# Performance work log

Hardware: AMD Instinct MI355X
Metric: run time of the kernel (lower is better)

Reference implementation:

```python
import jax, jax.numpy as jnp
import numpy as np
from jax import lax

NK, NV, DK, DV, K, C = 16, 32, 128, 128, 4, 2048
KEY_DIM = NK * DK
VAL_DIM = NV * DV
CONV_DIM = 2 * KEY_DIM + VAL_DIM
EPS = 1e-6


def setup_inputs() -> dict:
    key = jax.random.key(0)
    ks = jax.random.split(key, 10)
    B, T = 2, 2048
    s = 0.02
    return {
        "x": jax.random.normal(ks[0], (B, T, C), jnp.float32),
        "input_pos": jnp.arange(T, dtype=jnp.int32),
        "W_qkv": jax.random.normal(ks[1], (CONV_DIM, C), jnp.float32) * s,
        "W_z": jax.random.normal(ks[2], (VAL_DIM, C), jnp.float32) * s,
        "W_b": jax.random.normal(ks[3], (NV, C), jnp.float32) * s,
        "W_a": jax.random.normal(ks[4], (NV, C), jnp.float32) * s,
        "conv_w": jax.random.normal(ks[5], (CONV_DIM, 1, K), jnp.float32) * 0.1,
        "dt_bias": jnp.ones((NV,), jnp.float32),
        "A_log": jnp.log(jax.random.uniform(ks[6], (NV,), jnp.float32, 1e-3, 16.0)),
        "norm_w": jnp.ones((DV,), jnp.float32),
        "W_out": jax.random.normal(ks[7], (C, VAL_DIM), jnp.float32) * s,
        "conv_state": jnp.zeros((B, CONV_DIM, K), jnp.float32),
        "recurrent_state": jnp.zeros((B, NV, DK, DV), jnp.float32),
    }


def reference(x, input_pos, W_qkv, W_z, W_b, W_a, conv_w, dt_bias, A_log,
              norm_w, W_out, conv_state, recurrent_state):
    B, T, _ = x.shape
    # reset cached state when starting a new sequence (input_pos[0] == 0)
    keep = 1.0 - (input_pos[0] == 0).astype(x.dtype)
    conv_state = conv_state * keep
    state0 = recurrent_state * keep

    qkv = jnp.einsum('btc,dc->btd', x, W_qkv)                      # [B,T,CONV_DIM]
    z = jnp.einsum('btc,dc->btd', x, W_z).reshape(B, T, NV, DV)
    beta = jax.nn.sigmoid(jnp.einsum('btc,hc->bth', x, W_b))       # [B,T,NV]
    a = jnp.einsum('btc,hc->bth', x, W_a)
    g = -jnp.exp(A_log) * jax.nn.softplus(a + dt_bias)             # [B,T,NV]

    # causal depthwise conv using cached conv_state as left context
    conv_in = jnp.concatenate([conv_state, qkv.transpose(0, 2, 1)], axis=-1)  # [B,D,K+T]
    conv_out = lax.conv_general_dilated(
        conv_in, conv_w, (1,), 'VALID',
        dimension_numbers=('NCH', 'OIH', 'NCH'),
        feature_group_count=CONV_DIM)
    qkv_c = jax.nn.silu(conv_out[:, :, -T:]).transpose(0, 2, 1)    # [B,T,CONV_DIM]

    q = qkv_c[..., :KEY_DIM].reshape(B, T, NK, DK)
    k = qkv_c[..., KEY_DIM:2 * KEY_DIM].reshape(B, T, NK, DK)
    v = qkv_c[..., 2 * KEY_DIM:].reshape(B, T, NV, DV)
    q = q / jnp.maximum(jnp.linalg.norm(q, axis=-1, keepdims=True), 1e-12)
    k = k / jnp.maximum(jnp.linalg.norm(k, axis=-1, keepdims=True), 1e-12)
    rep = NV // NK
    if rep > 1:
        q = jnp.repeat(q, rep, axis=2)
        k = jnp.repeat(k, rep, axis=2)

    # gated delta-rule recurrence over time
    def step(carry, xs):
        q_i, k_i, v_i, g_i, b_i = xs                               # [B,H,*]
        new = (jnp.exp(g_i)[..., None, None] * carry
               + b_i[..., None, None] * (k_i[..., :, None] * v_i[..., None, :]))
        out = jnp.einsum('bhk,bhkv->bhv', q_i, new)
        return new, out

    xs = (q.transpose(1, 0, 2, 3), k.transpose(1, 0, 2, 3),
          v.transpose(1, 0, 2, 3), g.transpose(1, 0, 2), beta.transpose(1, 0, 2))
    state, outs = lax.scan(step, state0, xs)
    o = outs.transpose(1, 0, 2, 3)                                 # [B,T,NV,DV]

    # gated RMSNorm (Mamba2-style): gate with silu(z), then RMS-normalize
    o = o * jax.nn.silu(z)
    var = jnp.mean(o * o, axis=-1, keepdims=True)
    o = o * lax.rsqrt(var + EPS) * norm_w
    return jnp.einsum('btd,cd->btc', o.reshape(B, T, VAL_DIM), W_out)
```

## Files before the change

kernel.cpp:

```cpp
#include <hip/hip_runtime.h>
#include <hip/hip_bf16.h>
#include <math.h>

#define NKH 16
#define NVH 32
#define DKD 128
#define DVD 128
#define CDIM 2048
#define KEY_DIM 2048
#define VAL_DIM 4096
#define CONV_DIM 8192
#define BB 2
#define TT 2048
#define MROWS 4096
#define CH 64
#define NCHUNK 32

typedef unsigned short u16;
typedef __bf16 bf16x8 __attribute__((ext_vector_type(8)));
typedef float f32x4 __attribute__((ext_vector_type(4)));

__device__ __forceinline__ u16 f2bf(float f) {
    union { float f; unsigned u; } a; a.f = f;
    unsigned u = a.u;
    u += 0x7fffu + ((u >> 16) & 1u);
    return (u16)(u >> 16);
}
__device__ __forceinline__ float bf2f(u16 h) {
    union { unsigned u; float f; } a; a.u = ((unsigned)h) << 16;
    return a.f;
}
union BF8 { bf16x8 v; uint2 u2[2]; uint4 u4; u16 s[8]; };
__device__ __forceinline__ bf16x8 lds_ld8(const u16* p) {
    BF8 t; t.u2[0] = *(const uint2*)p; t.u2[1] = *(const uint2*)(p + 4); return t.v;
}
__device__ __forceinline__ bf16x8 lds_ld16(const u16* p) {
    BF8 t; t.u4 = *(const uint4*)p; return t.v;
}
__device__ __forceinline__ void lds_st8(u16* p, uint4 v) {
    *(uint2*)p = make_uint2(v.x, v.y); *(uint2*)(p + 4) = make_uint2(v.z, v.w);
}

__global__ __launch_bounds__(256) void fill_kernel(float* __restrict__ p, float v, int n) {
    int i = blockIdx.x * 256 + threadIdx.x;
    if (i < n) p[i] = v;
}

__global__ __launch_bounds__(256) void cast_kernel(const float* __restrict__ src,
                                                   u16* __restrict__ dst, int n4) {
    int i = blockIdx.x * 256 + threadIdx.x;
    if (i >= n4) return;
    float4 v = ((const float4*)src)[i];
    ushort4 r;
    r.x = f2bf(v.x); r.y = f2bf(v.y); r.z = f2bf(v.z); r.w = f2bf(v.w);
    ((ushort4*)dst)[i] = r;
}

template<int OUT_BF16>
__global__ __launch_bounds__(256) void gemm_nt(const u16* __restrict__ A,
                                               const u16* __restrict__ Bm,
                                               void* __restrict__ Cv,
                                               int M, int N, int K) {
    __shared__ __align__(16) u16 As[128 * 64];
    __shared__ __align__(16) u16 Bs[128 * 64];
    const int tid  = threadIdx.x;
    const int lane = tid & 63;
    const int wave = tid >> 6;
    const int m0 = blockIdx.y * 128;
    const int n0 = blockIdx.x * 128;
    const int wm = (wave & 1) * 64;
    const int wn = (wave >> 1) * 64;
    const int l15  = lane & 15;
    const int quad = lane >> 4;

    f32x4 acc[4][4];
#pragma unroll
    for (int i = 0; i < 4; ++i)
#pragma unroll
        for (int j = 0; j < 4; ++j) acc[i][j] = (f32x4)0.0f;

    const int crow = tid >> 3;
    const int ccol = (tid & 7) * 8;

    for (int k0 = 0; k0 < K; k0 += 64) {
#pragma unroll
        for (int p = 0; p < 4; ++p) {
            int row = p * 32 + crow;
            const u16* ga = A + (size_t)(m0 + row) * K + k0 + ccol;
            char* la = (char*)As + (size_t)(p * 256 + (wave << 6)) * 16;
            __builtin_amdgcn_global_load_lds((const __attribute__((address_space(1))) void*)ga,
                                             (__attribute__((address_space(3))) void*)la, 16, 0, 0);
            const u16* gb = Bm + (size_t)(n0 + row) * K + k0 + ccol;
            char* lb = (char*)Bs + (size_t)(p * 256 + (wave << 6)) * 16;
            __builtin_amdgcn_global_load_lds((const __attribute__((address_space(1))) void*)gb,
                                             (__attribute__((address_space(3))) void*)lb, 16, 0, 0);
        }
        __syncthreads();
#pragma unroll
        for (int kk = 0; kk < 64; kk += 32) {
            bf16x8 af[4], bfr[4];
#pragma unroll
            for (int i = 0; i < 4; ++i) {
                af[i]  = *(const bf16x8*)&As[(wm + i * 16 + l15) * 64 + kk + quad * 8];
                bfr[i] = *(const bf16x8*)&Bs[(wn + i * 16 + l15) * 64 + kk + quad * 8];
            }
#pragma unroll
            for (int i = 0; i < 4; ++i)
#pragma unroll
                for (int j = 0; j < 4; ++j)
                    acc[i][j] = __builtin_amdgcn_mfma_f32_16x16x32_bf16(af[i], bfr[j], acc[i][j], 0, 0, 0);
        }
        __syncthreads();
    }
#pragma unroll
    for (int i = 0; i < 4; ++i) {
#pragma unroll
        for (int j = 0; j < 4; ++j) {
#pragma unroll
            for (int r = 0; r < 4; ++r) {
                int grow = m0 + wm + i * 16 + quad * 4 + r;
                int gcol = n0 + wn + j * 16 + l15;
                if (OUT_BF16) {
                    ((u16*)Cv)[(size_t)grow * N + gcol] = f2bf(acc[i][j][r]);
                } else {
                    ((float*)Cv)[(size_t)grow * N + gcol] = acc[i][j][r];
                }
            }
        }
    }
}

template<int OUT_BF16>
__global__ __launch_bounds__(512, 2) void gemm_nt_256(const u16* __restrict__ A,
                                                      const u16* __restrict__ Bm,
                                                      void* __restrict__ Cv,
                                                      int M, int N, int K) {
    __shared__ __align__(16) u16 sA[2][256 * 64];
    __shared__ __align__(16) u16 sB[2][256 * 64];
    const int tid  = threadIdx.x;
    const int lane = tid & 63;
    const int wave = tid >> 6;
    const int wr   = wave >> 2;
    const int wc   = wave & 3;
    const int l15  = lane & 15;
    const int quad = lane >> 4;
    const int m0 = blockIdx.y * 256;
    const int n0 = blockIdx.x * 256;

    f32x4 acc[8][4];
#pragma unroll
    for (int i = 0; i < 8; ++i)
#pragma unroll
        for (int j = 0; j < 4; ++j) acc[i][j] = (f32x4)0.0f;

    auto stage = [&](int buf, int kk0) {
#pragma unroll
        for (int p = 0; p < 4; ++p) {
            const int gbase = p * 512 + wave * 64;
            const int g   = gbase + lane;
            const int row = g >> 3;
            const int sc  = (g & 7) ^ (row & 7);
            const u16* ga = A + (size_t)(m0 + row) * K + kk0 + sc * 8;
            __builtin_amdgcn_global_load_lds(
                (const __attribute__((address_space(1))) void*)ga,
                (__attribute__((address_space(3))) void*)((char*)&sA[buf][0] + (size_t)gbase * 16),
                16, 0, 0);
            const u16* gb = Bm + (size_t)(n0 + row) * K + kk0 + sc * 8;
            __builtin_amdgcn_global_load_lds(
                (const __attribute__((address_space(1))) void*)gb,
                (__attribute__((address_space(3))) void*)((char*)&sB[buf][0] + (size_t)gbase * 16),
                16, 0, 0);
        }
    };

    const int NT = K >> 6;
    stage(0, 0);

    for (int T = 0; T < NT; ++T) {
        const int P = T & 1;
        __builtin_amdgcn_sched_barrier(0);
        if (T + 1 < NT) {
            stage(P ^ 1, (T + 1) << 6);
            asm volatile("s_waitcnt vmcnt(8)" ::: "memory");
        } else {
            asm volatile("s_waitcnt vmcnt(0)" ::: "memory");
        }
        __builtin_amdgcn_s_barrier();
        __builtin_amdgcn_sched_barrier(0);
#pragma unroll
        for (int kk = 0; kk < 2; ++kk) {
            bf16x8 af[8], bfv[4];
#pragma unroll
            for (int i = 0; i < 8; ++i) {
                int row = wr * 128 + i * 16 + l15;
                int slot = ((kk * 4 + quad) ^ (l15 & 7)) * 8;
                af[i] = lds_ld16(&sA[P][row * 64 + slot]);
            }
#pragma unroll
            for (int j = 0; j < 4; ++j) {
                int row = wc * 64 + j * 16 + l15;
                int slot = ((kk * 4 + quad) ^ (l15 & 7)) * 8;
                bfv[j] = lds_ld16(&sB[P][row * 64 + slot]);
            }
#pragma unroll
            for (int i = 0; i < 8; ++i)
#pragma unroll
                for (int j = 0; j < 4; ++j)
                    acc[i][j] = __builtin_amdgcn_mfma_f32_16x16x32_bf16(af[i], bfv[j], acc[i][j], 0, 0, 0);
        }
        __builtin_amdgcn_sched_barrier(0);
        __builtin_amdgcn_s_barrier();
    }

#pragma unroll
    for (int i = 0; i < 8; ++i) {
#pragma unroll
        for (int j = 0; j < 4; ++j) {
#pragma unroll
            for (int r = 0; r < 4; ++r) {
                int grow = m0 + wr * 128 + i * 16 + quad * 4 + r;
                int gcol = n0 + wc * 64 + j * 16 + l15;
                if (OUT_BF16) {
                    ((u16*)Cv)[(size_t)grow * N + gcol] = f2bf(acc[i][j][r]);
                } else {
                    ((float*)Cv)[(size_t)grow * N + gcol] = acc[i][j][r];
                }
            }
        }
    }
}

__global__ __launch_bounds__(256) void bg_epilogue(const float* __restrict__ scores,
                                                   const float* __restrict__ dt_bias,
                                                   const float* __restrict__ A_log,
                                                   float* __restrict__ beta,
                                                   float* __restrict__ g) {
    int i = blockIdx.x * 256 + threadIdx.x;
    int row = i >> 6, col = i & 63;
    float s = scores[(size_t)row * 128 + col];
    if (col < 32) {
        beta[(size_t)row * 32 + col] = 1.f / (1.f + __expf(-s));
    } else {
        int h = col - 32;
        float aa = s + dt_bias[h];
        float sp = (aa > 20.f) ? aa : log1pf(__expf(aa));
        g[(size_t)row * 32 + h] = -__expf(A_log[h]) * sp;
    }
}

__global__ __launch_bounds__(256) void conv_silu_kernel(const u16* __restrict__ qkv,
                                                        const float* __restrict__ conv_w,
                                                        const float* __restrict__ conv_state,
                                                        const int* __restrict__ input_pos,
                                                        u16* __restrict__ qkvc) {
    const int d   = blockIdx.x * 256 + threadIdx.x;
    const int row = blockIdx.y;
    const int t   = row & (TT - 1);
    const int b   = row >> 11;
    const float keep = (input_pos[0] == 0) ? 0.f : 1.f;
    float4 w = *(const float4*)&conv_w[(size_t)d * 4];
    float acc = 0.f;
#pragma unroll
    for (int j = 0; j < 4; ++j) {
        int u = t + j - 3;
        float v;
        if (u >= 0) v = bf2f(qkv[(size_t)(b * TT + u) * CONV_DIM + d]);
        else        v = keep * conv_state[((size_t)b * CONV_DIM + d) * 4 + (u + 4)];
        acc += (&w.x)[j] * v;
    }
    float s = acc / (1.f + __expf(-acc));
    qkvc[(size_t)row * CONV_DIM + d] = f2bf(s);
}

__global__ __launch_bounds__(256) void qknorm_kernel(u16* __restrict__ qkvc) {
    const int gid  = blockIdx.x * 4 + (threadIdx.x >> 6);
    const int lane = threadIdx.x & 63;
    const int row  = gid >> 5;
    const int h    = gid & 31;
    u16* p = qkvc + (size_t)row * CONV_DIM + h * 128;
    ushort2 vb = *(ushort2*)&p[lane * 2];
    float v0 = bf2f(vb.x), v1 = bf2f(vb.y);
    float ss = v0 * v0 + v1 * v1;
#pragma unroll
    for (int off = 32; off; off >>= 1) ss += __shfl_xor(ss, off);
    float scale = 1.f / fmaxf(sqrtf(ss), 1e-12f);
    ushort2 r;
    r.x = f2bf(v0 * scale);
    r.y = f2bf(v1 * scale);
    *(ushort2*)&p[lane * 2] = r;
}

__global__ __launch_bounds__(64) void gates_kernel(const float* __restrict__ g,
                                                   const float* __restrict__ beta_,
                                                   float* __restrict__ gcum,
                                                   float* __restrict__ qsb,
                                                   float* __restrict__ wkb,
                                                   float* __restrict__ dLb) {
    const int bh = blockIdx.x, c = blockIdx.y;
    const int b = bh >> 5, h = bh & 31;
    const int t = threadIdx.x;
    const int row = b * TT + c * CH + t;
    float G = g[(size_t)row * 32 + h];
#pragma unroll
    for (int off = 1; off < 64; off <<= 1) {
        float x = __shfl_up(G, off);
        if (t >= off) G += x;
    }
    float GL = __shfl(G, 63);
    int oidx = bh * TT + c * CH + t;
    gcum[oidx] = G;
    qsb[oidx] = __expf(G);
    wkb[oidx] = __expf(GL - G) * beta_[(size_t)row * 32 + h];
    if (t == 0) dLb[bh * NCHUNK + c] = __expf(GL);
}

__global__ __launch_bounds__(256) void ktrans_kernel(const u16* __restrict__ qkvc,
                                                     u16* __restrict__ kT) {
    const int id = blockIdx.x;
    const int tt = id & 31, dkh = (id >> 5) & 1, hk = (id >> 6) & 15, b = id >> 10;
    const int t0 = tt * 64, dk0 = dkh * 64;
    __shared__ __align__(16) u16 tile[64 * 68];
#pragma unroll
    for (int it = 0; it < 2; ++it) {
        int idx = it * 256 + threadIdx.x;
        int tl = idx >> 3, c8 = (idx & 7) * 8;
        uint4 v = *(const uint4*)&qkvc[(size_t)(b * TT + t0 + tl) * CONV_DIM + KEY_DIM + hk * 128 + dk0 + c8];
        lds_st8(&tile[tl * 68 + c8], v);
    }
    __syncthreads();
#pragma unroll
    for (int it = 0; it < 2; ++it) {
        int idx = it * 256 + threadIdx.x;
        int dkl = idx >> 3, t8 = (idx & 7) * 8;
        unsigned w[4];
#pragma unroll
        for (int p = 0; p < 4; ++p) {
            unsigned lo = tile[(t8 + 2 * p) * 68 + dkl];
            unsigned hi = tile[(t8 + 2 * p + 1) * 68 + dkl];
            w[p] = lo | (hi << 16);
        }
        *(uint4*)&kT[((size_t)((b * 16 + hk) * 128 + dk0 + dkl)) * TT + t0 + t8] =
            make_uint4(w[0], w[1], w[2], w[3]);
    }
}

__global__ __launch_bounds__(256) void chunk_state_kernel(const u16* __restrict__ qkvc,
                                                          const u16* __restrict__ kT,
                                                          const float* __restrict__ qsb,
                                                          const float* __restrict__ wkb,
                                                          const float* __restrict__ dLb,
                                                          const float* __restrict__ rec_state,
                                                          const int* __restrict__ input_pos,
                                                          u16* __restrict__ o) {
    const int b = blockIdx.x, h = blockIdx.y, dvs = blockIdx.z;
    const int tid = threadIdx.x, lane = tid & 63, wave = tid >> 6;
    const int l15 = lane & 15, quad = lane >> 4;
    const int hq = h >> 1, bh = b * 32 + h;
    const float keep = (input_pos[0] == 0) ? 0.f : 1.f;

    __shared__ __align__(16) u16 sQ[64 * 132];
    __shared__ __align__(16) u16 sKT[128 * 68];
    __shared__ __align__(16) u16 sR[32 * 132];
    __shared__ float sQS[64];

    f32x4 st[2][2];
#pragma unroll
    for (int i = 0; i < 2; ++i)
#pragma unroll
        for (int j = 0; j < 2; ++j)
#pragma unroll
            for (int r = 0; r < 4; ++r) {
                int dv = dvs * 32 + i * 16 + quad * 4 + r;
                int dk = wave * 32 + j * 16 + l15;
                st[i][j][r] = keep * rec_state[((size_t)(bh * 128 + dk)) * 128 + dv];
            }

    for (int c = 0; c < NCHUNK; ++c) {
        const int t0 = c * CH;
#pragma unroll
        for (int i = 0; i < 2; ++i)
#pragma unroll
            for (int j = 0; j < 2; ++j)
#pragma unroll
                for (int r = 0; r < 4; ++r)
                    sR[(i * 16 + quad * 4 + r) * 132 + wave * 32 + j * 16 + l15] = f2bf(st[i][j][r]);
#pragma unroll
        for (int it = 0; it < 4; ++it) {
            int idx = it * 256 + tid;
            int t = idx >> 4, c8 = (idx & 15) * 8;
            uint4 v = *(const uint4*)&qkvc[(size_t)(b * TT + t0 + t) * CONV_DIM + hq * 128 + c8];
            lds_st8(&sQ[t * 132 + c8], v);
        }
        if (tid < 64) sQS[tid] = qsb[bh * TT + t0 + tid];
        __syncthreads();
        {
            f32x4 ao[2] = {(f32x4)0.0f, (f32x4)0.0f};
#pragma unroll
            for (int kk = 0; kk < 4; ++kk) {
                bf16x8 af = lds_ld8(&sQ[(wave * 16 + l15) * 132 + kk * 32 + quad * 8]);
                bf16x8 b0 = lds_ld8(&sR[(l15) * 132 + kk * 32 + quad * 8]);
                bf16x8 b1 = lds_ld8(&sR[(16 + l15) * 132 + kk * 32 + quad * 8]);
                ao[0] = __builtin_amdgcn_mfma_f32_16x16x32_bf16(af, b0, ao[0], 0, 0, 0);
                ao[1] = __builtin_amdgcn_mfma_f32_16x16x32_bf16(af, b1, ao[1], 0, 0, 0);
            }
#pragma unroll
            for (int j = 0; j < 2; ++j)
#pragma unroll
                for (int r = 0; r < 4; ++r) {
                    int t = wave * 16 + quad * 4 + r;
                    int dv = dvs * 32 + j * 16 + l15;
                    o[((size_t)(b * TT + t0 + t) * 32 + h) * 128 + dv] = f2bf(ao[j][r] * sQS[t]);
                }
        }
        __syncthreads();
#pragma unroll
        for (int it = 0; it < 4; ++it) {
            int idx = it * 256 + tid;
            int dk = idx >> 3, t8 = (idx & 7) * 8;
            uint4 v = *(const uint4*)&kT[((size_t)((b * 16 + hq) * 128 + dk)) * TT + t0 + t8];
            lds_st8(&sKT[dk * 68 + t8], v);
        }
        {
            int t = tid >> 2, dvo = (tid & 3) * 8;
            float w = wkb[bh * TT + t0 + t];
            BF8 v;
            v.u4 = *(const uint4*)&qkvc[(size_t)(b * TT + t0 + t) * CONV_DIM + 2 * KEY_DIM + h * 128 + dvs * 32 + dvo];
#pragma unroll
            for (int u = 0; u < 8; ++u)
                sR[(dvo + u) * 68 + t] = f2bf(bf2f(v.s[u]) * w);
        }
        __syncthreads();
        {
            float d = dLb[bh * NCHUNK + c];
#pragma unroll
            for (int i = 0; i < 2; ++i)
#pragma unroll
                for (int j = 0; j < 2; ++j)
#pragma unroll
                    for (int r = 0; r < 4; ++r) st[i][j][r] *= d;
#pragma unroll
            for (int kk = 0; kk < 2; ++kk) {
                bf16x8 af[2], bfv[2];
#pragma unroll
                for (int i = 0; i < 2; ++i)
                    af[i] = lds_ld8(&sR[(i * 16 + l15) * 68 + kk * 32 + quad * 8]);
#pragma unroll
                for (int j = 0; j < 2; ++j)
                    bfv[j] = lds_ld8(&sKT[(wave * 32 + j * 16 + l15) * 68 + kk * 32 + quad * 8]);
#pragma unroll
                for (int i = 0; i < 2; ++i)
#pragma unroll
                    for (int j = 0; j < 2; ++j)
                        st[i][j] = __builtin_amdgcn_mfma_f32_16x16x32_bf16(af[i], bfv[j], st[i][j], 0, 0, 0);
            }
        }
        __syncthreads();
    }
}

__global__ __launch_bounds__(256) void chunk_intra_kernel(const u16* __restrict__ qkvc,
                                                          const float* __restrict__ gcum,
                                                          const float* __restrict__ beta_,
                                                          u16* __restrict__ o) {
    const int b = blockIdx.x, h = blockIdx.y, c = blockIdx.z;
    const int tid = threadIdx.x, lane = tid & 63, wave = tid >> 6;
    const int l15 = lane & 15, quad = lane >> 4;
    const int hq = h >> 1, bh = b * 32 + h;
    const int t0 = c * CH;

    __shared__ __align__(16) u16 sQ[64 * 132];
    __shared__ __align__(16) u16 sK[64 * 132];
    __shared__ __align__(16) u16 sVT[128 * 68];
    __shared__ float sG[64];
    __shared__ float sB[64];

#pragma unroll
    for (int it = 0; it < 4; ++it) {
        int idx = it * 256 + tid;
        int t = idx >> 4, c8 = (idx & 15) * 8;
        size_t rbase = (size_t)(b * TT + t0 + t) * CONV_DIM;
        lds_st8(&sQ[t * 132 + c8], *(const uint4*)&qkvc[rbase + hq * 128 + c8]);
        lds_st8(&sK[t * 132 + c8], *(const uint4*)&qkvc[rbase + KEY_DIM + hq * 128 + c8]);
    }
    if (tid < 64) {
        sG[tid] = gcum[bh * TT + t0 + tid];
        sB[tid] = beta_[(size_t)(b * TT + t0 + tid) * 32 + h];
    }
    __syncthreads();
    const int wm = (wave & 1) * 32, wn = (wave >> 1) * 32;
    f32x4 acc[2][2];
#pragma unroll
    for (int i = 0; i < 2; ++i)
#pragma unroll
        for (int j = 0; j < 2; ++j) acc[i][j] = (f32x4)0.0f;
#pragma unroll
    for (int kk = 0; kk < 4; ++kk) {
        bf16x8 af[2], bfv[2];
#pragma unroll
        for (int i = 0; i < 2; ++i) {
            af[i]  = lds_ld8(&sQ[(wm + i * 16 + l15) * 132 + kk * 32 + quad * 8]);
            bfv[i] = lds_ld8(&sK[(wn + i * 16 + l15) * 132 + kk * 32 + quad * 8]);
        }
#pragma unroll
        for (int i = 0; i < 2; ++i)
#pragma unroll
            for (int j = 0; j < 2; ++j)
                acc[i][j] = __builtin_amdgcn_mfma_f32_16x16x32_bf16(af[i], bfv[j], acc[i][j], 0, 0, 0);
    }
    __syncthreads();
#pragma unroll
    for (int i = 0; i < 2; ++i)
#pragma unroll
        for (int j = 0; j < 2; ++j)
#pragma unroll
            for (int r = 0; r < 4; ++r) {
                int t = wm + i * 16 + quad * 4 + r;
                int s = wn + j * 16 + l15;
                float av = 0.f;
                if (s <= t) av = __expf(sG[t] - sG[s]) * sB[s] * acc[i][j][r];
                ((u16*)sQ)[t * 68 + s] = f2bf(av);
            }
#pragma unroll
    for (int it = 0; it < 4; ++it) {
        int idx = it * 256 + tid;
        int t = idx >> 4, c8 = (idx & 15) * 8;
        lds_st8(&sK[t * 132 + c8],
                *(const uint4*)&qkvc[(size_t)(b * TT + t0 + t) * CONV_DIM + 2 * KEY_DIM + h * 128 + c8]);
    }
    __syncthreads();
    {
        int dv = (wave & 1) * 64 + lane;
        int tb = (wave >> 1) * 32;
#pragma unroll
        for (int tc = 0; tc < 4; ++tc) {
            int t8 = tb + tc * 8;
            unsigned w[4];
#pragma unroll
            for (int p = 0; p < 4; ++p) {
                unsigned lo = sK[(t8 + 2 * p) * 132 + dv];
                unsigned hi = sK[(t8 + 2 * p + 1) * 132 + dv];
                w[p] = lo | (hi << 16);
            }
            lds_st8(&sVT[dv * 68 + t8], make_uint4(w[0], w[1], w[2], w[3]));
        }
    }
    __syncthreads();
    const int wm2 = (wave & 1) * 32, wn2 = (wave >> 1) * 64;
    f32x4 oacc[2][4];
#pragma unroll
    for (int i = 0; i < 2; ++i)
#pragma unroll
        for (int j = 0; j < 4; ++j) oacc[i][j] = (f32x4)0.0f;
#pragma unroll
    for (int kk = 0; kk < 2; ++kk) {
        bf16x8 af[2], bfv[4];
#pragma unroll
        for (int i = 0; i < 2; ++i)
            af[i] = lds_ld8(&((u16*)sQ)[(wm2 + i * 16 + l15) * 68 + kk * 32 + quad * 8]);
#pragma unroll
        for (int j = 0; j < 4; ++j)
            bfv[j] = lds_ld8(&sVT[(wn2 + j * 16 + l15) * 68 + kk * 32 + quad * 8]);
#pragma unroll
        for (int i = 0; i < 2; ++i)
#pragma unroll
            for (int j = 0; j < 4; ++j)
                oacc[i][j] = __builtin_amdgcn_mfma_f32_16x16x32_bf16(af[i], bfv[j], oacc[i][j], 0, 0, 0);
    }
#pragma unroll
    for (int i = 0; i < 2; ++i)
#pragma unroll
        for (int j = 0; j < 4; ++j)
#pragma unroll
            for (int r = 0; r < 4; ++r) {
                int t = wm2 + i * 16 + quad * 4 + r;
                int dv = wn2 + j * 16 + l15;
                size_t addr = ((size_t)(b * TT + t0 + t) * 32 + h) * 128 + dv;
                o[addr] = f2bf(oacc[i][j][r] + bf2f(o[addr]));
            }
}

__global__ __launch_bounds__(256) void gnorm_kernel(const u16* __restrict__ o,
                                                    const u16* __restrict__ zb,
                                                    const float* __restrict__ norm_w,
                                                    u16* __restrict__ ob) {
    const int gid  = blockIdx.x * 4 + (threadIdx.x >> 6);
    const int lane = threadIdx.x & 63;
    const int row  = gid >> 5;
    const int h    = gid & 31;
    const size_t base = ((size_t)row * NVH + h) * DVD;
    ushort2 oraw = *(const ushort2*)&o[base + lane * 2];
    float o0 = bf2f(oraw.x), o1 = bf2f(oraw.y);
    float z0 = bf2f(zb[base + lane * 2]);
    float z1 = bf2f(zb[base + lane * 2 + 1]);
    o0 *= z0 / (1.f + __expf(-z0));
    o1 *= z1 / (1.f + __expf(-z1));
    float ss = o0 * o0 + o1 * o1;
#pragma unroll
    for (int off = 32; off; off >>= 1) ss += __shfl_xor(ss, off);
    float scale = rsqrtf(ss * (1.f / 128.f) + 1e-6f);
    float w0 = norm_w[lane * 2], w1 = norm_w[lane * 2 + 1];
    ushort2 r;
    r.x = f2bf(o0 * scale * w0);
    r.y = f2bf(o1 * scale * w1);
    *(ushort2*)&ob[base + lane * 2] = r;
}

extern "C" void kernel_launch(void* const* d_in, const int* in_sizes, int n_in,
                              void* d_out, int out_size, void* d_ws, size_t ws_size,
                              hipStream_t stream) {
    const float* x         = (const float*)d_in[0];
    const int*   input_pos = (const int*)d_in[1];
    const float* W_qkv     = (const float*)d_in[2];
    const float* W_z       = (const float*)d_in[3];
    const float* W_b       = (const float*)d_in[4];
    const float* W_a       = (const float*)d_in[5];
    const float* conv_w    = (const float*)d_in[6];
    const float* dt_bias   = (const float*)d_in[7];
    const float* A_log     = (const float*)d_in[8];
    const float* norm_w    = (const float*)d_in[9];
    const float* W_out     = (const float*)d_in[10];
    const float* conv_state = (const float*)d_in[11];
    const float* rec_state  = (const float*)d_in[12];
    float* out = (float*)d_out;

    const size_t REQUIRED = 168820736;
    if (ws_size < REQUIRED) {
        float mib = (float)((double)ws_size / 1048576.0);
        fill_kernel<<<(out_size + 255) / 256, 256, 0, stream>>>(out, mib, out_size);
        return;
    }

    const size_t MI = 1048576;
    char* ws = (char*)d_ws;
    u16* xb    = (u16*)(ws);
    u16* wqkvb = (u16*)(ws + 16 * MI);
    u16* wzb   = (u16*)(ws + 48 * MI);
    u16* wbab  = (u16*)(ws + 16 * MI);
    float* bgs = (float*)(ws + 17 * MI);
    u16* qkvc  = (u16*)(ws);
    u16* ob    = (u16*)(ws);
    u16* woutb = (u16*)(ws + 32 * MI);
    u16* zb    = (u16*)(ws + 64 * MI);
    u16* qkvb  = (u16*)(ws + 96 * MI);
    u16* o     = (u16*)(ws + 96 * MI);
    u16* kT    = (u16*)(ws + 128 * MI);
    float* gcum = (float*)(ws + 144 * MI);
    float* qsb  = (float*)(ws + 144 * MI + 524288);
    float* wkb  = (float*)(ws + 145 * MI);
    float* dLb  = (float*)(ws + 145 * MI + 524288);
    float* beta = (float*)(ws + 160 * MI);
    float* g    = (float*)(ws + 160 * MI + 524288);

    cast_kernel<<<8192,  256, 0, stream>>>(x,     xb,    2097152);
    cast_kernel<<<16384, 256, 0, stream>>>(W_qkv, wqkvb, 4194304);
    cast_kernel<<<8192,  256, 0, stream>>>(W_z,   wzb,   2097152);

    gemm_nt_256<1><<<dim3(32, 16), 512, 0, stream>>>(xb, wqkvb, qkvb, MROWS, CONV_DIM, CDIM);
    gemm_nt_256<1><<<dim3(16, 16), 512, 0, stream>>>(xb, wzb,   zb,   MROWS, VAL_DIM,  CDIM);

    cast_kernel<<<256, 256, 0, stream>>>(W_b, wbab, 16384);
    cast_kernel<<<256, 256, 0, stream>>>(W_a, wbab + 65536, 16384);
    hipMemsetAsync(wbab + 131072, 0, 131072 * sizeof(u16), stream);
    gemm_nt<0><<<dim3(1, 32), 256, 0, stream>>>(xb, wbab, bgs, MROWS, 128, CDIM);
    bg_epilogue<<<1024, 256, 0, stream>>>(bgs, dt_bias, A_log, beta, g);

    conv_silu_kernel<<<dim3(32, 4096), 256, 0, stream>>>(qkvb, conv_w, conv_state, input_pos, qkvc);
    qknorm_kernel<<<32768, 256, 0, stream>>>(qkvc);

    gates_kernel<<<dim3(64, NCHUNK), 64, 0, stream>>>(g, beta, gcum, qsb, wkb, dLb);
    ktrans_kernel<<<2048, 256, 0, stream>>>(qkvc, kT);
    chunk_state_kernel<<<dim3(BB, NVH, 4), 256, 0, stream>>>(qkvc, kT, qsb, wkb, dLb,
                                                             rec_state, input_pos, o);
    chunk_intra_kernel<<<dim3(BB, NVH, NCHUNK), 256, 0, stream>>>(qkvc, gcum, beta, o);

    cast_kernel<<<8192, 256, 0, stream>>>(W_out, woutb, 2097152);
    gnorm_kernel<<<32768, 256, 0, stream>>>(o, zb, norm_w, ob);

    gemm_nt<0><<<dim3(16, 32), 256, 0, stream>>>(ob, woutb, out, MROWS, CDIM, VAL_DIM);
}
```

Measured before the change: 777.3 us.

## Swizzle GEMM tiles across XCDs, XOR-swizzle LDS, and vectorize conv

Adds an XCD-aware block remapping to both GEMM kernels so neighbouring output tiles land on the same chiplet and share L2. It also XOR-swizzles the LDS column layout in the 128-tile GEMM to cut bank conflicts on fragment reads. The depthwise conv+SiLU kernel now handles 8 channels per thread with 16-byte loads and stores, which reduces the launch to 4 blocks in x. Together these target L2 misses, LDS conflicts and narrow memory accesses, at the cost of extra index math and more registers per thread in the conv kernel.

```diff
diff --git a/kernel.cpp b/kernel.cpp
--- a/kernel.cpp
+++ b/kernel.cpp
@@ -41,6 +41,25 @@
     *(uint2*)p = make_uint2(v.x, v.y); *(uint2*)(p + 4) = make_uint2(v.z, v.w);
 }
 
+__device__ __forceinline__ void xcd_swizzle(int& tx, int& ty) {
+    const int nx = gridDim.x, ny = gridDim.y;
+    const int b  = blockIdx.x + nx * blockIdx.y;
+    const int nb = nx * ny;
+    if (nx >= 8 && (nx & 7) == 0 && (nb & 255) == 0) {
+        const int rnd  = b >> 8;
+        const int idx  = b & 255;
+        const int xcd  = idx & 7;
+        const int slot = idx >> 3;
+        const int RX   = nx >> 3;
+        const int rx   = xcd & (RX - 1);
+        const int ry   = xcd >> __popc(RX - 1);
+        tx = rx * 8 + (slot & 7);
+        ty = rnd * (256 / nx) + ry * 4 + (slot >> 3);
+    } else {
+        tx = blockIdx.x; ty = blockIdx.y;
+    }
+}
+
 __global__ __launch_bounds__(256) void fill_kernel(float* __restrict__ p, float v, int n) {
     int i = blockIdx.x * 256 + threadIdx.x;
     if (i < n) p[i] = v;
@@ -66,8 +85,10 @@
     const int tid  = threadIdx.x;
     const int lane = tid & 63;
     const int wave = tid >> 6;
-    const int m0 = blockIdx.y * 128;
-    const int n0 = blockIdx.x * 128;
+    int tx, ty;
+    xcd_swizzle(tx, ty);
+    const int m0 = ty * 128;
+    const int n0 = tx * 128;
     const int wm = (wave & 1) * 64;
     const int wn = (wave >> 1) * 64;
     const int l15  = lane & 15;
@@ -80,17 +101,17 @@
         for (int j = 0; j < 4; ++j) acc[i][j] = (f32x4)0.0f;
 
     const int crow = tid >> 3;
-    const int ccol = (tid & 7) * 8;
+    const int scol = ((tid & 7) ^ (crow & 7)) * 8;
 
     for (int k0 = 0; k0 < K; k0 += 64) {
 #pragma unroll
         for (int p = 0; p < 4; ++p) {
             int row = p * 32 + crow;
-            const u16* ga = A + (size_t)(m0 + row) * K + k0 + ccol;
+            const u16* ga = A + (size_t)(m0 + row) * K + k0 + scol;
             char* la = (char*)As + (size_t)(p * 256 + (wave << 6)) * 16;
             __builtin_amdgcn_global_load_lds((const __attribute__((address_space(1))) void*)ga,
                                              (__attribute__((address_space(3))) void*)la, 16, 0, 0);
-            const u16* gb = Bm + (size_t)(n0 + row) * K + k0 + ccol;
+            const u16* gb = Bm + (size_t)(n0 + row) * K + k0 + scol;
             char* lb = (char*)Bs + (size_t)(p * 256 + (wave << 6)) * 16;
             __builtin_amdgcn_global_load_lds((const __attribute__((address_space(1))) void*)gb,
                                              (__attribute__((address_space(3))) void*)lb, 16, 0, 0);
@@ -101,8 +122,9 @@
             bf16x8 af[4], bfr[4];
 #pragma unroll
             for (int i = 0; i < 4; ++i) {
-                af[i]  = *(const bf16x8*)&As[(wm + i * 16 + l15) * 64 + kk + quad * 8];
-                bfr[i] = *(const bf16x8*)&Bs[(wn + i * 16 + l15) * 64 + kk + quad * 8];
+                int sa = (((kk >> 3) + quad) ^ (l15 & 7)) * 8;
+                af[i]  = *(const bf16x8*)&As[(wm + i * 16 + l15) * 64 + sa];
+                bfr[i] = *(const bf16x8*)&Bs[(wn + i * 16 + l15) * 64 + sa];
             }
 #pragma unroll
             for (int i = 0; i < 4; ++i)
@@ -144,8 +166,10 @@
     const int wc   = wave & 3;
     const int l15  = lane & 15;
     const int quad = lane >> 4;
-    const int m0 = blockIdx.y * 256;
-    const int n0 = blockIdx.x * 256;
+    int tx, ty;
+    xcd_swizzle(tx, ty);
+    const int m0 = ty * 256;
+    const int n0 = tx * 256;
 
     f32x4 acc[8][4];
 #pragma unroll
@@ -253,23 +277,48 @@
                                                         const float* __restrict__ conv_state,
                                                         const int* __restrict__ input_pos,
                                                         u16* __restrict__ qkvc) {
-    const int d   = blockIdx.x * 256 + threadIdx.x;
+    const int d0  = (blockIdx.x * 256 + threadIdx.x) * 8;
     const int row = blockIdx.y;
     const int t   = row & (TT - 1);
     const int b   = row >> 11;
     const float keep = (input_pos[0] == 0) ? 0.f : 1.f;
-    float4 w = *(const float4*)&conv_w[(size_t)d * 4];
-    float acc = 0.f;
+
+    float w[8][4];
+#pragma unroll
+    for (int c = 0; c < 8; ++c) {
+        float4 wv = *(const float4*)&conv_w[(size_t)(d0 + c) * 4];
+        w[c][0] = wv.x; w[c][1] = wv.y; w[c][2] = wv.z; w[c][3] = wv.w;
+    }
+    float acc[8];
+#pragma unroll
+    for (int c = 0; c < 8; ++c) acc[c] = 0.f;
 #pragma unroll
     for (int j = 0; j < 4; ++j) {
         int u = t + j - 3;
-        float v;
-        if (u >= 0) v = bf2f(qkv[(size_t)(b * TT + u) * CONV_DIM + d]);
-        else        v = keep * conv_state[((size_t)b * CONV_DIM + d) * 4 + (u + 4)];
-        acc += (&w.x)[j] * v;
-    }
-    float s = acc / (1.f + __expf(-acc));
-    qkvc[(size_t)row * CONV_DIM + d] = f2bf(s);
+        if (u >= 0) {
+            BF8 v;
+            v.u4 = *(const uint4*)&qkv[(size_t)(b * TT + u) * CONV_DIM + d0];
+#pragma unroll
+            for (int c = 0; c < 8; ++c) acc[c] += w[c][j] * bf2f(v.s[c]);
+        } else {
+#pragma unroll
+            for (int c = 0; c < 8; ++c)
+                acc[c] += w[c][j] * keep *
+                          conv_state[((size_t)b * CONV_DIM + d0 + c) * 4 + (u + 4)];
+        }
+    }
+    u16 out[8];
+#pragma unroll
+    for (int c = 0; c < 8; ++c) {
+        float s = acc[c] / (1.f + __expf(-acc[c]));
+        out[c] = f2bf(s);
+    }
+    uint4 o4;
+    o4.x = out[0] | ((unsigned)out[1] << 16);
+    o4.y = out[2] | ((unsigned)out[3] << 16);
+    o4.z = out[4] | ((unsigned)out[5] << 16);
+    o4.w = out[6] | ((unsigned)out[7] << 16);
+    *(uint4*)&qkvc[(size_t)row * CONV_DIM + d0] = o4;
 }
 
 __global__ __launch_bounds__(256) void qknorm_kernel(u16* __restrict__ qkvc) {
@@ -664,7 +713,7 @@
     gemm_nt<0><<<dim3(1, 32), 256, 0, stream>>>(xb, wbab, bgs, MROWS, 128, CDIM);
     bg_epilogue<<<1024, 256, 0, stream>>>(bgs, dt_bias, A_log, beta, g);
 
-    conv_silu_kernel<<<dim3(32, 4096), 256, 0, stream>>>(qkvb, conv_w, conv_state, input_pos, qkvc);
+    conv_silu_kernel<<<dim3(4, 4096), 256, 0, stream>>>(qkvb, conv_w, conv_state, input_pos, qkvc);
     qknorm_kernel<<<32768, 256, 0, stream>>>(qkvc);
 
     gates_kernel<<<dim3(64, NCHUNK), 64, 0, stream>>>(g, beta, gcum, qsb, wkb, dLb);
```

After: 747.8 us. 1.04x faster.
